# Optimization experiments

Hardware: AMD Instinct MI355X
Metric: run time of the kernel (lower is better)

## Reference

```python
import jax, jax.numpy as jnp
import numpy as np

# Dims: N nodes, C channels (multiplicity), K = 9 input spherical comps (l=0,1,2),
# E elements, output irreps L in {0,1} with M_L = 2L+1, correlation nu = 3.
N, C, K, E = 1024, 128, 9, 10
M = {0: 1, 1: 3}
P = {1: 1, 2: 2, 3: 3}  # number of symmetric-contraction paths per correlation order


def setup_inputs() -> dict:
    key = jax.random.key(0)
    ks = iter(jax.random.split(key, 32))
    inp = {}
    inp["node_feats"] = jax.random.normal(next(ks), (N, C, K), jnp.float32)
    species = jax.random.randint(next(ks), (N,), 0, E)
    inp["node_attrs"] = jax.nn.one_hot(species, E, dtype=jnp.float32)
    inp["sc"] = jax.random.normal(next(ks), (N, C * (M[0] + M[1])), jnp.float32)
    # Generalized CG coefficient tensors U_t (fixed basis; random stand-ins with
    # the same shape/contraction structure as the real Clebsch-Gordan U matrices)
    # and learned element-dependent weights W_t, per output irrep L.
    for L in (0, 1):
        for t in (1, 2, 3):
            u = jax.random.normal(next(ks), (K,) * t + (M[L], P[t]), jnp.float32)
            inp[f"U{t}_{L}"] = u * (K ** (-0.5 * t))
            inp[f"W{t}_{L}"] = jax.random.normal(next(ks), (E, P[t], C), jnp.float32) / np.sqrt(P[t])
        inp[f"Wlin_{L}"] = jax.random.normal(next(ks), (C, C), jnp.float32)
    return inp


def _sym_contract(x, na, U1, U2, U3, W1, W2, W3):
    # x: [N,C,K] node features, na: [N,E] one-hot element attrs.
    # Per-node path weights: [N,P_t,C]
    w1 = jnp.einsum('ne,epc->npc', na, W1)
    w2 = jnp.einsum('ne,epc->npc', na, W2)
    w3 = jnp.einsum('ne,epc->npc', na, W3)
    # Horner-style recursion of MACE's Contraction (highest order first):
    out = jnp.einsum('ijkmp,npc,nck->ncmij', U3, w3, x)      # [N,C,M,K,K]
    ct = jnp.einsum('ijmp,npc->ncmij', U2, w2) + out
    out = jnp.einsum('ncmij,ncj->ncmi', ct, x)               # [N,C,M,K]
    ct = jnp.einsum('imp,npc->ncmi', U1, w1) + out
    out = jnp.einsum('ncmi,nci->ncm', ct, x)                 # [N,C,M]
    return out


def reference(node_feats, node_attrs, sc,
              U1_0, U2_0, U3_0, U1_1, U2_1, U3_1,
              W1_0, W2_0, W3_0, W1_1, W2_1, W3_1,
              Wlin_0, Wlin_1):
    y0 = _sym_contract(node_feats, node_attrs, U1_0, U2_0, U3_0, W1_0, W2_0, W3_0)  # [N,C,1]
    y1 = _sym_contract(node_feats, node_attrs, U1_1, U2_1, U3_1, W1_1, W2_1, W3_1)  # [N,C,3]
    inv = 1.0 / np.sqrt(node_feats.shape[1])  # e3nn Linear fan-in normalization
    z0 = jnp.einsum('ncm,cd->ndm', y0, Wlin_0) * inv
    z1 = jnp.einsum('ncm,cd->ndm', y1, Wlin_1) * inv
    n = node_feats.shape[0]
    out = jnp.concatenate([z0.reshape(n, -1), z1.reshape(n, -1)], axis=-1)  # [N, 512]
    return out + sc
```

## Files before the change

### kernel.cpp

```cpp
#include <hip/hip_runtime.h>


typedef __attribute__((ext_vector_type(8))) short short8;
typedef __attribute__((ext_vector_type(16))) float f32x16;

#define NSTEP 14
#define TBLB_DWORDS (NSTEP*64*4)
#define WL_OFF TBLB_DWORDS
#define TBLW_DWORDS (64*256)

static __device__ __forceinline__ short bf16b(float f) {
  __bf16 h = (__bf16)f;
  return __builtin_bit_cast(short, h);
}

struct Triples { unsigned char a[224], b[224], c3[224], ord[224]; };
constexpr Triples make_triples() {
  Triples T{};
  int s = 0;
  for (int i = 0; i < 9; ++i)
    for (int j = i; j < 9; ++j)
      for (int k = j; k < 9; ++k) { T.a[s]=(unsigned char)i; T.b[s]=(unsigned char)j; T.c3[s]=(unsigned char)k; T.ord[s]=3; ++s; }
  for (int i = 0; i < 9; ++i)
    for (int j = i; j < 9; ++j) { T.a[s]=(unsigned char)i; T.b[s]=(unsigned char)j; T.ord[s]=2; ++s; }
  for (int i = 0; i < 9; ++i) { T.a[s]=(unsigned char)i; T.ord[s]=1; ++s; }
  for (; s < 224; ++s) T.ord[s] = 0;
  return T;
}
static constexpr Triples TRI = make_triples();

struct DecTab {
  unsigned short b3[165][6]; unsigned char c3[165];
  unsigned short b2[45][2];  unsigned char c2[45];
};
constexpr DecTab make_dectab() {
  DecTab D{};
  int s = 0;
  for (int i = 0; i < 9; ++i)
    for (int j = i; j < 9; ++j)
      for (int k = j; k < 9; ++k) {
        int pm[6][3] = {{i,j,k},{i,k,j},{j,i,k},{j,k,i},{k,i,j},{k,j,i}};
        int cnt = 0;
        for (int q = 0; q < 6; ++q) {
          bool dup = false;
          for (int r = 0; r < q; ++r)
            if (pm[r][0]==pm[q][0] && pm[r][1]==pm[q][1] && pm[r][2]==pm[q][2]) dup = true;
          if (!dup) { D.b3[s][cnt] = (unsigned short)((pm[q][0]*9 + pm[q][1])*9 + pm[q][2]); ++cnt; }
        }
        D.c3[s] = (unsigned char)cnt; ++s;
      }
  s = 0;
  for (int i = 0; i < 9; ++i)
    for (int j = i; j < 9; ++j) {
      D.b2[s][0] = (unsigned short)(i*9 + j);
      D.b2[s][1] = (unsigned short)(j*9 + i);
      D.c2[s] = (unsigned char)((i == j) ? 1 : 2); ++s;
    }
  return D;
}
static constexpr DecTab DT = make_dectab();

template<int KI>
static __device__ __forceinline__ float monoT(const float* xr) {
  if constexpr (TRI.ord[KI] == 3) return xr[TRI.a[KI]] * xr[TRI.b[KI]] * xr[TRI.c3[KI]];
  else if constexpr (TRI.ord[KI] == 2) return xr[TRI.a[KI]] * xr[TRI.b[KI]];
  else if constexpr (TRI.ord[KI] == 1) return xr[TRI.a[KI]];
  else return 0.f;
}

template<int K0>
static __device__ __forceinline__ void mono8(const float* xr, float m[8]) {
  m[0]=monoT<K0+0>(xr); m[1]=monoT<K0+1>(xr); m[2]=monoT<K0+2>(xr); m[3]=monoT<K0+3>(xr);
  m[4]=monoT<K0+4>(xr); m[5]=monoT<K0+5>(xr); m[6]=monoT<K0+6>(xr); m[7]=monoT<K0+7>(xr);
}

template<int T>
static __device__ __forceinline__ void k_steps(const float* xr, const unsigned int* __restrict__ tbl,
                                               int lane, int ks, f32x16& acc) {
  if constexpr (T < NSTEP) {
    float m[8];
    if (ks == 0) mono8<T*16>(xr, m);
    else         mono8<T*16 + 8>(xr, m);
    short8 mf;
    mf[0]=bf16b(m[0]); mf[1]=bf16b(m[1]); mf[2]=bf16b(m[2]); mf[3]=bf16b(m[3]);
    mf[4]=bf16b(m[4]); mf[5]=bf16b(m[5]); mf[6]=bf16b(m[6]); mf[7]=bf16b(m[7]);
    short8 cf = *(const short8*)&tbl[(T*64 + lane)*4];
    acc = __builtin_amdgcn_mfma_f32_32x32x16_bf16(cf, mf, acc, 0, 0, 0);
    k_steps<T+1>(xr, tbl, lane, ks, acc);
  }
}

static __device__ __forceinline__ float coefval(int k, int col,
    const float* U1_0, const float* U2_0, const float* U3_0,
    const float* U1_1, const float* U2_1, const float* U3_1) {
  if (k < 165) {
    if (col < 12 || col >= 24) return 0.f;
    int mp = (col - 12) / 3, p = (col - 12) % 3;
    float acc = 0.f;
    int cnt = DT.c3[k];
    for (int q = 0; q < cnt; ++q) {
      int base = DT.b3[k][q];
      acc += (mp == 0) ? U3_0[base*3 + p] : U3_1[base*9 + (mp-1)*3 + p];
    }
    return acc;
  } else if (k < 210) {
    if (col < 4 || col >= 12) return 0.f;
    int mp = (col - 4) / 2, p = (col - 4) % 2;
    int s2 = k - 165;
    float acc = 0.f;
    int cnt = DT.c2[s2];
    for (int q = 0; q < cnt; ++q) {
      int base = DT.b2[s2][q];
      acc += (mp == 0) ? U2_0[base*2 + p] : U2_1[(base*3 + (mp-1))*2 + p];
    }
    return acc;
  } else if (k < 219) {
    int i = k - 210;
    if (col == 0) return U1_0[i];
    if (col < 4) return U1_1[i*3 + (col-1)];
    return 0.f;
  }
  return 0.f;
}

__global__ __launch_bounds__(64) void build_tables_kernel(
    const float* __restrict__ U1_0, const float* __restrict__ U2_0, const float* __restrict__ U3_0,
    const float* __restrict__ U1_1, const float* __restrict__ U2_1, const float* __restrict__ U3_1,
    const float* __restrict__ Wl0, const float* __restrict__ Wl1,
    unsigned int* __restrict__ tbl) {
  const int b = blockIdx.x, l = threadIdx.x;
  const int col = l & 31, ks = l >> 5;
  if (b < NSTEP) {
    const int ft = b;
    #pragma unroll
    for (int d = 0; d < 4; ++d) {
      int k = ft*16 + ks*8 + d*2;
      unsigned short lo = (unsigned short)bf16b(coefval(k,   col, U1_0,U2_0,U3_0,U1_1,U2_1,U3_1));
      unsigned short hi = (unsigned short)bf16b(coefval(k+1, col, U1_0,U2_0,U3_0,U1_1,U2_1,U3_1));
      tbl[(ft*64 + l)*4 + d] = ((unsigned int)hi << 16) | lo;
    }
  } else {
    const int u = b - NSTEP;
    const int g = u >> 5, u5 = u & 31, nt = u5 >> 3, st = u5 & 7;
    const float* W = g ? Wl1 : Wl0;
    #pragma unroll
    for (int d = 0; d < 4; ++d) {
      int k = st*16 + ks*8 + 2*d;
      unsigned short lo = (unsigned short)bf16b(W[(long)k*128     + nt*32 + col]);
      unsigned short hi = (unsigned short)bf16b(W[(long)(k+1)*128 + nt*32 + col]);
      tbl[WL_OFF + u*256 + l*4 + d] = ((unsigned int)hi << 16) | lo;
    }
  }
}

__global__ __launch_bounds__(512, 4) void epbb_mfma_kernel(
    const float* __restrict__ xg,
    const float* __restrict__ na,
    const float* __restrict__ sc,
    const float* __restrict__ W1_0, const float* __restrict__ W2_0, const float* __restrict__ W3_0,
    const float* __restrict__ W1_1, const float* __restrict__ W2_1, const float* __restrict__ W3_1,
    const unsigned int* __restrict__ tbl,
    float* __restrict__ out) {
  __shared__ __align__(16) short lds_yA[2][8][136];

  const int tid  = threadIdx.x;
  const int lane = tid & 63;
  const int w    = tid >> 6;
  const int ks   = lane >> 5;
  const int n0   = blockIdx.x * 2;

  const int nw = w >> 2;
  const int n  = n0 + nw;
  const int c0 = (w & 3) * 32;
  const int cl = c0 + (lane & 31);
  const float* xp = xg + ((long)(n*128 + cl))*9;
  float xr[9];
  #pragma unroll
  for (int q = 0; q < 9; ++q) xr[q] = xp[q];

  int e = 0;
  #pragma unroll
  for (int q = 0; q < 10; ++q) e = (na[(long)n*10 + q] > 0.5f) ? q : e;

  const float w10  = W1_0[e*128 + cl];
  const float w20a = W2_0[(e*2+0)*128 + cl], w20b = W2_0[(e*2+1)*128 + cl];
  const float w30a = W3_0[(e*3+0)*128 + cl], w30b = W3_0[(e*3+1)*128 + cl], w30c = W3_0[(e*3+2)*128 + cl];
  const float w11  = W1_1[e*128 + cl];
  const float w21a = W2_1[(e*2+0)*128 + cl], w21b = W2_1[(e*2+1)*128 + cl];
  const float w31a = W3_1[(e*3+0)*128 + cl], w31b = W3_1[(e*3+1)*128 + cl], w31c = W3_1[(e*3+2)*128 + cl];

  f32x16 acc;
  #pragma unroll
  for (int q = 0; q < 16; ++q) acc[q] = 0.f;

  k_steps<0>(xr, tbl, lane, ks, acc);

  float p0, p1, p2, p3;
  if (ks == 0) {
    p0 = w10*acc[0];
    p1 = w11*acc[1] + w31b*acc[8]  + w31c*acc[9];
    p2 = w11*acc[2] + w21a*acc[4]  + w21b*acc[5] + w31a*acc[10] + w31b*acc[11];
    p3 = w11*acc[3] + w21a*acc[6]  + w21b*acc[7];
  } else {
    p0 = w20a*acc[0] + w20b*acc[1] + w30a*acc[4] + w30b*acc[5] + w30c*acc[6];
    p1 = w21a*acc[2] + w21b*acc[3] + w31a*acc[7];
    p2 = w31c*acc[8];
    p3 = w31a*acc[9] + w31b*acc[10] + w31c*acc[11];
  }
  const float y0 = p0 + __shfl_xor(p0, 32, 64);
  const float y1 = p1 + __shfl_xor(p1, 32, 64);
  const float y2 = p2 + __shfl_xor(p2, 32, 64);
  const float y3 = p3 + __shfl_xor(p3, 32, 64);

  if (ks == 0) {
    lds_yA[0][nw][cl]     = bf16b(y0);
    lds_yA[1][nw][cl]     = bf16b(y1);
  } else {
    lds_yA[1][2 + nw][cl] = bf16b(y2);
    lds_yA[1][4 + nw][cl] = bf16b(y3);
  }
  __syncthreads();

  const int g  = w >> 2;
  const int nt = w & 3;
  f32x16 z;
  #pragma unroll
  for (int q = 0; q < 16; ++q) z[q] = 0.f;
  const unsigned int* bw = tbl + WL_OFF + ((g*4 + nt)*8)*256;
  #pragma unroll
  for (int st = 0; st < 8; ++st) {
    short8 af = *(const short8*)&lds_yA[g][lane & 7][st*16 + ks*8];
    short8 bf = *(const short8*)&bw[st*256 + lane*4];
    z = __builtin_amdgcn_mfma_f32_32x32x16_bf16(af, bf, z, 0, 0, 0);
  }
  const float inv = 0.088388347648318447f;
  const int d = nt*32 + (lane & 31);
  if (g == 0) {
    if (ks == 0) {
      #pragma unroll
      for (int r = 0; r < 2; ++r) {
        long o = (long)(n0 + r)*512 + d;
        out[o] = z[r]*inv + sc[o];
      }
    }
  } else {
    if (ks == 0) {
      #pragma unroll
      for (int r = 0; r < 4; ++r) {
        long o = (long)(n0 + (r & 1))*512 + 128 + 3*d + (r >> 1);
        out[o] = z[r]*inv + sc[o];
      }
    } else {
      #pragma unroll
      for (int r = 0; r < 2; ++r) {
        long o = (long)(n0 + r)*512 + 128 + 3*d + 2;
        out[o] = z[r]*inv + sc[o];
      }
    }
  }
}

extern "C" void kernel_launch(void* const* d_in, const int* in_sizes, int n_in,
                              void* d_out, int out_size, void* d_ws, size_t ws_size,
                              hipStream_t stream) {
  const float* xg   = (const float*)d_in[0];
  const float* na   = (const float*)d_in[1];
  const float* sc   = (const float*)d_in[2];
  const float* U1_0 = (const float*)d_in[3];
  const float* W1_0 = (const float*)d_in[4];
  const float* U2_0 = (const float*)d_in[5];
  const float* W2_0 = (const float*)d_in[6];
  const float* U3_0 = (const float*)d_in[7];
  const float* W3_0 = (const float*)d_in[8];
  const float* Wl0  = (const float*)d_in[9];
  const float* U1_1 = (const float*)d_in[10];
  const float* W1_1 = (const float*)d_in[11];
  const float* U2_1 = (const float*)d_in[12];
  const float* W2_1 = (const float*)d_in[13];
  const float* U3_1 = (const float*)d_in[14];
  const float* W3_1 = (const float*)d_in[15];
  const float* Wl1  = (const float*)d_in[16];

  unsigned int* tbl = (unsigned int*)d_ws;
  const int N = in_sizes[0] / (128 * 9);

  hipLaunchKernelGGL(build_tables_kernel, dim3(NSTEP + 64), dim3(64), 0, stream,
                     U1_0, U2_0, U3_0, U1_1, U2_1, U3_1, Wl0, Wl1, tbl);
  hipLaunchKernelGGL(epbb_mfma_kernel, dim3(N/2), dim3(512), 0, stream,
                     xg, na, sc, W1_0, W2_0, W3_0, W1_1, W2_1, W3_1, tbl,
                     (float*)d_out);
}
```

Baseline: 25.64 us.

## Stage coefficient table and inputs in LDS, coalesce output stores

The coefficient B-table is copied into shared memory once per block, so the MFMA operand loads read LDS instead of global memory. Node features are loaded with coalesced float4 copies into LDS rather than 9 strided scalar loads per thread. The output is gathered in LDS and written together with the sc residual as coalesced float4 stores instead of scattered scalar writes. This adds about 14KB of LDS per block and extra barriers, which may reduce occupancy.

```diff
diff --git a/kernel.cpp b/kernel.cpp
--- a/kernel.cpp
+++ b/kernel.cpp
@@ -75,7 +75,7 @@
 }
 
 template<int T>
-static __device__ __forceinline__ void k_steps(const float* xr, const unsigned int* __restrict__ tbl,
+static __device__ __forceinline__ void k_steps(const float* xr, const unsigned int* lds_b,
                                                int lane, int ks, f32x16& acc) {
   if constexpr (T < NSTEP) {
     float m[8];
@@ -84,9 +84,9 @@
     short8 mf;
     mf[0]=bf16b(m[0]); mf[1]=bf16b(m[1]); mf[2]=bf16b(m[2]); mf[3]=bf16b(m[3]);
     mf[4]=bf16b(m[4]); mf[5]=bf16b(m[5]); mf[6]=bf16b(m[6]); mf[7]=bf16b(m[7]);
-    short8 cf = *(const short8*)&tbl[(T*64 + lane)*4];
+    short8 cf = *(const short8*)&lds_b[(T*64 + lane)*4];
     acc = __builtin_amdgcn_mfma_f32_32x32x16_bf16(cf, mf, acc, 0, 0, 0);
-    k_steps<T+1>(xr, tbl, lane, ks, acc);
+    k_steps<T+1>(xr, lds_b, lane, ks, acc);
   }
 }
 
@@ -161,7 +161,10 @@
     const float* __restrict__ W1_1, const float* __restrict__ W2_1, const float* __restrict__ W3_1,
     const unsigned int* __restrict__ tbl,
     float* __restrict__ out) {
+  __shared__ __align__(16) unsigned int lds_b[TBLB_DWORDS];
+  __shared__ __align__(16) float lds_x[2*128*9];
   __shared__ __align__(16) short lds_yA[2][8][136];
+  __shared__ __align__(16) float lds_out[2*512];
 
   const int tid  = threadIdx.x;
   const int lane = tid & 63;
@@ -169,14 +172,18 @@
   const int ks   = lane >> 5;
   const int n0   = blockIdx.x * 2;
 
+  for (int q = tid; q < TBLB_DWORDS; q += 512) lds_b[q] = tbl[q];
+  {
+    const float4* xg4 = (const float4*)(xg + (long)n0*1152);
+    float4* lx4 = (float4*)lds_x;
+    #pragma unroll
+    for (int q = tid; q < 576; q += 512) lx4[q] = xg4[q];
+  }
+
   const int nw = w >> 2;
   const int n  = n0 + nw;
   const int c0 = (w & 3) * 32;
   const int cl = c0 + (lane & 31);
-  const float* xp = xg + ((long)(n*128 + cl))*9;
-  float xr[9];
-  #pragma unroll
-  for (int q = 0; q < 9; ++q) xr[q] = xp[q];
 
   int e = 0;
   #pragma unroll
@@ -189,11 +196,20 @@
   const float w21a = W2_1[(e*2+0)*128 + cl], w21b = W2_1[(e*2+1)*128 + cl];
   const float w31a = W3_1[(e*3+0)*128 + cl], w31b = W3_1[(e*3+1)*128 + cl], w31c = W3_1[(e*3+2)*128 + cl];
 
+  __syncthreads();
+
+  float xr[9];
+  {
+    const float* myx = lds_x + (nw*128 + cl)*9;
+    #pragma unroll
+    for (int q = 0; q < 9; ++q) xr[q] = myx[q];
+  }
+
   f32x16 acc;
   #pragma unroll
   for (int q = 0; q < 16; ++q) acc[q] = 0.f;
 
-  k_steps<0>(xr, tbl, lane, ks, acc);
+  k_steps<0>(xr, lds_b, lane, ks, acc);
 
   float p0, p1, p2, p3;
   if (ks == 0) {
@@ -237,26 +253,27 @@
   const int d = nt*32 + (lane & 31);
   if (g == 0) {
     if (ks == 0) {
-      #pragma unroll
-      for (int r = 0; r < 2; ++r) {
-        long o = (long)(n0 + r)*512 + d;
-        out[o] = z[r]*inv + sc[o];
-      }
+      lds_out[0*512 + d] = z[0]*inv;
+      lds_out[1*512 + d] = z[1]*inv;
     }
   } else {
     if (ks == 0) {
-      #pragma unroll
-      for (int r = 0; r < 4; ++r) {
-        long o = (long)(n0 + (r & 1))*512 + 128 + 3*d + (r >> 1);
-        out[o] = z[r]*inv + sc[o];
-      }
+      lds_out[0*512 + 128 + 3*d + 0] = z[0]*inv;
+      lds_out[1*512 + 128 + 3*d + 0] = z[1]*inv;
+      lds_out[0*512 + 128 + 3*d + 1] = z[2]*inv;
+      lds_out[1*512 + 128 + 3*d + 1] = z[3]*inv;
     } else {
-      #pragma unroll
-      for (int r = 0; r < 2; ++r) {
-        long o = (long)(n0 + r)*512 + 128 + 3*d + 2;
-        out[o] = z[r]*inv + sc[o];
-      }
-    }
+      lds_out[0*512 + 128 + 3*d + 2] = z[0]*inv;
+      lds_out[1*512 + 128 + 3*d + 2] = z[1]*inv;
+    }
+  }
+  __syncthreads();
+
+  if (tid < 256) {
+    float4 v = ((const float4*)lds_out)[tid];
+    float4 s = *(const float4*)(sc + (long)n0*512 + tid*4);
+    v.x += s.x; v.y += s.y; v.z += s.z; v.w += s.w;
+    *(float4*)(out + (long)n0*512 + tid*4) = v;
   }
 }
 
```

Measured after the change: 25.36 us. About the same (-1.1%).

## Process four nodes per block, stage coefficient table and skip in LDS

Applied to the files above, without the earlier changes.

Each block now handles four nodes instead of two. Each wave computes two 32-channel tiles, so the output linear MFMA runs on fuller A rows (4 or 16 rows instead of 2 or 8). The 14-step coefficient table is copied once into LDS and the MFMA B operands are read from there rather than global memory. The skip tensor is prefetched into LDS with vector loads. This amortises table loads and the linear-layer weights over more nodes, at the cost of more LDS, more registers, lower occupancy bounds and half as many blocks.

```diff
diff --git a/kernel.cpp b/kernel.cpp
--- a/kernel.cpp
+++ b/kernel.cpp
@@ -5,6 +5,7 @@
 typedef __attribute__((ext_vector_type(16))) float f32x16;
 
 #define NSTEP 14
+#define NODES 4
 #define TBLB_DWORDS (NSTEP*64*4)
 #define WL_OFF TBLB_DWORDS
 #define TBLW_DWORDS (64*256)
@@ -75,7 +76,7 @@
 }
 
 template<int T>
-static __device__ __forceinline__ void k_steps(const float* xr, const unsigned int* __restrict__ tbl,
+static __device__ __forceinline__ void k_steps(const float* xr, const unsigned int* lds_b,
                                                int lane, int ks, f32x16& acc) {
   if constexpr (T < NSTEP) {
     float m[8];
@@ -84,9 +85,43 @@
     short8 mf;
     mf[0]=bf16b(m[0]); mf[1]=bf16b(m[1]); mf[2]=bf16b(m[2]); mf[3]=bf16b(m[3]);
     mf[4]=bf16b(m[4]); mf[5]=bf16b(m[5]); mf[6]=bf16b(m[6]); mf[7]=bf16b(m[7]);
-    short8 cf = *(const short8*)&tbl[(T*64 + lane)*4];
+    short8 cf = *(const short8*)&lds_b[(T*64 + lane)*4];
     acc = __builtin_amdgcn_mfma_f32_32x32x16_bf16(cf, mf, acc, 0, 0, 0);
-    k_steps<T+1>(xr, tbl, lane, ks, acc);
+    k_steps<T+1>(xr, lds_b, lane, ks, acc);
+  }
+}
+
+struct PathW { float w10,w20a,w20b,w30a,w30b,w30c,w11,w21a,w21b,w31a,w31b,w31c; };
+
+static __device__ __forceinline__ void process_tile(
+    const float* xr, const PathW& W, const unsigned int* lds_b,
+    short* yA0, short* yA1, int lane, int ks, int nd, int cl) {
+  f32x16 acc;
+  #pragma unroll
+  for (int q = 0; q < 16; ++q) acc[q] = 0.f;
+  k_steps<0>(xr, lds_b, lane, ks, acc);
+  float p0, p1, p2, p3;
+  if (ks == 0) {
+    p0 = W.w10*acc[0];
+    p1 = W.w11*acc[1] + W.w31b*acc[8]  + W.w31c*acc[9];
+    p2 = W.w11*acc[2] + W.w21a*acc[4]  + W.w21b*acc[5] + W.w31a*acc[10] + W.w31b*acc[11];
+    p3 = W.w11*acc[3] + W.w21a*acc[6]  + W.w21b*acc[7];
+  } else {
+    p0 = W.w20a*acc[0] + W.w20b*acc[1] + W.w30a*acc[4] + W.w30b*acc[5] + W.w30c*acc[6];
+    p1 = W.w21a*acc[2] + W.w21b*acc[3] + W.w31a*acc[7];
+    p2 = W.w31c*acc[8];
+    p3 = W.w31a*acc[9] + W.w31b*acc[10] + W.w31c*acc[11];
+  }
+  const float y0 = p0 + __shfl_xor(p0, 32, 64);
+  const float y1 = p1 + __shfl_xor(p1, 32, 64);
+  const float y2 = p2 + __shfl_xor(p2, 32, 64);
+  const float y3 = p3 + __shfl_xor(p3, 32, 64);
+  if (ks == 0) {
+    yA0[nd*136 + cl]       = bf16b(y0);
+    yA1[nd*136 + cl]       = bf16b(y1);
+  } else {
+    yA1[(4+nd)*136 + cl]   = bf16b(y2);
+    yA1[(8+nd)*136 + cl]   = bf16b(y3);
   }
 }
 
@@ -153,7 +188,7 @@
   }
 }
 
-__global__ __launch_bounds__(512, 4) void epbb_mfma_kernel(
+__global__ __launch_bounds__(512, 2) void epbb_mfma_kernel(
     const float* __restrict__ xg,
     const float* __restrict__ na,
     const float* __restrict__ sc,
@@ -161,64 +196,56 @@
     const float* __restrict__ W1_1, const float* __restrict__ W2_1, const float* __restrict__ W3_1,
     const unsigned int* __restrict__ tbl,
     float* __restrict__ out) {
-  __shared__ __align__(16) short lds_yA[2][8][136];
+  __shared__ __align__(16) unsigned int lds_b[TBLB_DWORDS];
+  __shared__ __align__(16) short lds_yA0[4*136];
+  __shared__ __align__(16) short lds_yA1[16*136];
+  __shared__ __align__(16) float lds_sc[NODES*512];
 
   const int tid  = threadIdx.x;
   const int lane = tid & 63;
   const int w    = tid >> 6;
   const int ks   = lane >> 5;
-  const int n0   = blockIdx.x * 2;
-
-  const int nw = w >> 2;
-  const int n  = n0 + nw;
-  const int c0 = (w & 3) * 32;
-  const int cl = c0 + (lane & 31);
-  const float* xp = xg + ((long)(n*128 + cl))*9;
-  float xr[9];
-  #pragma unroll
-  for (int q = 0; q < 9; ++q) xr[q] = xp[q];
+  const int n0   = blockIdx.x * NODES;
+
+  const int nd  = w >> 1;
+  const int n   = n0 + nd;
+  const int cla = (w & 1)*64 + (lane & 31);
+  const int clb = cla + 32;
+
+  float xrA[9], xrB[9];
+  {
+    const float* xpA = xg + ((long)(n*128 + cla))*9;
+    const float* xpB = xg + ((long)(n*128 + clb))*9;
+    #pragma unroll
+    for (int q = 0; q < 9; ++q) { xrA[q] = xpA[q]; xrB[q] = xpB[q]; }
+  }
+
+  for (int q = tid; q < TBLB_DWORDS; q += 512) lds_b[q] = tbl[q];
+  ((float4*)lds_sc)[tid] = ((const float4*)(sc + (long)n0*512))[tid];
 
   int e = 0;
   #pragma unroll
   for (int q = 0; q < 10; ++q) e = (na[(long)n*10 + q] > 0.5f) ? q : e;
 
-  const float w10  = W1_0[e*128 + cl];
-  const float w20a = W2_0[(e*2+0)*128 + cl], w20b = W2_0[(e*2+1)*128 + cl];
-  const float w30a = W3_0[(e*3+0)*128 + cl], w30b = W3_0[(e*3+1)*128 + cl], w30c = W3_0[(e*3+2)*128 + cl];
-  const float w11  = W1_1[e*128 + cl];
-  const float w21a = W2_1[(e*2+0)*128 + cl], w21b = W2_1[(e*2+1)*128 + cl];
-  const float w31a = W3_1[(e*3+0)*128 + cl], w31b = W3_1[(e*3+1)*128 + cl], w31c = W3_1[(e*3+2)*128 + cl];
-
-  f32x16 acc;
-  #pragma unroll
-  for (int q = 0; q < 16; ++q) acc[q] = 0.f;
-
-  k_steps<0>(xr, tbl, lane, ks, acc);
-
-  float p0, p1, p2, p3;
-  if (ks == 0) {
-    p0 = w10*acc[0];
-    p1 = w11*acc[1] + w31b*acc[8]  + w31c*acc[9];
-    p2 = w11*acc[2] + w21a*acc[4]  + w21b*acc[5] + w31a*acc[10] + w31b*acc[11];
-    p3 = w11*acc[3] + w21a*acc[6]  + w21b*acc[7];
-  } else {
-    p0 = w20a*acc[0] + w20b*acc[1] + w30a*acc[4] + w30b*acc[5] + w30c*acc[6];
-    p1 = w21a*acc[2] + w21b*acc[3] + w31a*acc[7];
-    p2 = w31c*acc[8];
-    p3 = w31a*acc[9] + w31b*acc[10] + w31c*acc[11];
-  }
-  const float y0 = p0 + __shfl_xor(p0, 32, 64);
-  const float y1 = p1 + __shfl_xor(p1, 32, 64);
-  const float y2 = p2 + __shfl_xor(p2, 32, 64);
-  const float y3 = p3 + __shfl_xor(p3, 32, 64);
-
-  if (ks == 0) {
-    lds_yA[0][nw][cl]     = bf16b(y0);
-    lds_yA[1][nw][cl]     = bf16b(y1);
-  } else {
-    lds_yA[1][2 + nw][cl] = bf16b(y2);
-    lds_yA[1][4 + nw][cl] = bf16b(y3);
-  }
+  PathW WA, WB;
+  WA.w10  = W1_0[e*128 + cla];              WB.w10  = W1_0[e*128 + clb];
+  WA.w20a = W2_0[(e*2+0)*128 + cla];        WB.w20a = W2_0[(e*2+0)*128 + clb];
+  WA.w20b = W2_0[(e*2+1)*128 + cla];        WB.w20b = W2_0[(e*2+1)*128 + clb];
+  WA.w30a = W3_0[(e*3+0)*128 + cla];        WB.w30a = W3_0[(e*3+0)*128 + clb];
+  WA.w30b = W3_0[(e*3+1)*128 + cla];        WB.w30b = W3_0[(e*3+1)*128 + clb];
+  WA.w30c = W3_0[(e*3+2)*128 + cla];        WB.w30c = W3_0[(e*3+2)*128 + clb];
+  WA.w11  = W1_1[e*128 + cla];              WB.w11  = W1_1[e*128 + clb];
+  WA.w21a = W2_1[(e*2+0)*128 + cla];        WB.w21a = W2_1[(e*2+0)*128 + clb];
+  WA.w21b = W2_1[(e*2+1)*128 + cla];        WB.w21b = W2_1[(e*2+1)*128 + clb];
+  WA.w31a = W3_1[(e*3+0)*128 + cla];        WB.w31a = W3_1[(e*3+0)*128 + clb];
+  WA.w31b = W3_1[(e*3+1)*128 + cla];        WB.w31b = W3_1[(e*3+1)*128 + clb];
+  WA.w31c = W3_1[(e*3+2)*128 + cla];        WB.w31c = W3_1[(e*3+2)*128 + clb];
+
+  __syncthreads();
+
+  process_tile(xrA, WA, lds_b, lds_yA0, lds_yA1, lane, ks, nd, cla);
+  process_tile(xrB, WB, lds_b, lds_yA0, lds_yA1, lane, ks, nd, clb);
+
   __syncthreads();
 
   const int g  = w >> 2;
@@ -227,9 +254,11 @@
   #pragma unroll
   for (int q = 0; q < 16; ++q) z[q] = 0.f;
   const unsigned int* bw = tbl + WL_OFF + ((g*4 + nt)*8)*256;
+  const short* yA = g ? lds_yA1 : lds_yA0;
+  const int arow = g ? (lane & 15) : (lane & 3);
   #pragma unroll
   for (int st = 0; st < 8; ++st) {
-    short8 af = *(const short8*)&lds_yA[g][lane & 7][st*16 + ks*8];
+    short8 af = *(const short8*)&yA[arow*136 + st*16 + ks*8];
     short8 bf = *(const short8*)&bw[st*256 + lane*4];
     z = __builtin_amdgcn_mfma_f32_32x32x16_bf16(af, bf, z, 0, 0, 0);
   }
@@ -238,23 +267,28 @@
   if (g == 0) {
     if (ks == 0) {
       #pragma unroll
-      for (int r = 0; r < 2; ++r) {
+      for (int r = 0; r < 4; ++r) {
         long o = (long)(n0 + r)*512 + d;
-        out[o] = z[r]*inv + sc[o];
+        out[o] = z[r]*inv + lds_sc[r*512 + d];
       }
     }
   } else {
     if (ks == 0) {
       #pragma unroll
       for (int r = 0; r < 4; ++r) {
-        long o = (long)(n0 + (r & 1))*512 + 128 + 3*d + (r >> 1);
-        out[o] = z[r]*inv + sc[o];
+        long o = (long)(n0 + r)*512 + 128 + 3*d + 0;
+        out[o] = z[r]*inv + lds_sc[r*512 + 128 + 3*d + 0];
+      }
+      #pragma unroll
+      for (int r = 4; r < 8; ++r) {
+        long o = (long)(n0 + (r-4))*512 + 128 + 3*d + 2;
+        out[o] = z[r]*inv + lds_sc[(r-4)*512 + 128 + 3*d + 2];
       }
     } else {
       #pragma unroll
-      for (int r = 0; r < 2; ++r) {
-        long o = (long)(n0 + r)*512 + 128 + 3*d + 2;
-        out[o] = z[r]*inv + sc[o];
+      for (int r = 0; r < 4; ++r) {
+        long o = (long)(n0 + r)*512 + 128 + 3*d + 1;
+        out[o] = z[r]*inv + lds_sc[r*512 + 128 + 3*d + 1];
       }
     }
   }
@@ -286,7 +320,7 @@
 
   hipLaunchKernelGGL(build_tables_kernel, dim3(NSTEP + 64), dim3(64), 0, stream,
                      U1_0, U2_0, U3_0, U1_1, U2_1, U3_1, Wl0, Wl1, tbl);
-  hipLaunchKernelGGL(epbb_mfma_kernel, dim3(N/2), dim3(512), 0, stream,
+  hipLaunchKernelGGL(epbb_mfma_kernel, dim3(N/NODES), dim3(512), 0, stream,
                      xg, na, sc, W1_0, W2_0, W3_0, W1_1, W2_1, W3_1, tbl,
                      (float*)d_out);
 }
```

Result: no change. 25.67 us (+0.1%).

## Fuse table build into main kernel with paired monomial packing and precomputed pair products

Applied to the files above, without the earlier changes.

Removes the separate table-building launch. Each block now builds the CG coefficient table in LDS, and the Wlin weights are converted to bf16 from global memory inside the output GEMM loop. Monomials are reordered into pairs that share a quadratic factor, so each MFMA lane reuses precomputed x_i*x_j products (P45) instead of recomputing triple products. In exchange, every one of the 512 blocks redoes the coefficient-table work and Wlin conversion. Register pressure also rises, and the occupancy hint drops from 4 to 2.

```diff
diff --git a/kernel.cpp b/kernel.cpp
--- a/kernel.cpp
+++ b/kernel.cpp
@@ -5,29 +5,68 @@
 typedef __attribute__((ext_vector_type(16))) float f32x16;
 
 #define NSTEP 14
+#define NPOS (NSTEP*8)
 #define TBLB_DWORDS (NSTEP*64*4)
-#define WL_OFF TBLB_DWORDS
-#define TBLW_DWORDS (64*256)
 
 static __device__ __forceinline__ short bf16b(float f) {
   __bf16 h = (__bf16)f;
   return __builtin_bit_cast(short, h);
 }
 
-struct Triples { unsigned char a[224], b[224], c3[224], ord[224]; };
-constexpr Triples make_triples() {
-  Triples T{};
-  int s = 0;
+constexpr int pidx(int i, int j) { return 9*i - i*(i-1)/2 + (j - i); }
+
+struct MonoGF { unsigned char g, f; };
+constexpr MonoGF mono_gf(int id) {
+  if (id < 165) {
+    int s = 0;
+    for (int i = 0; i < 9; ++i)
+      for (int j = i; j < 9; ++j)
+        for (int k = j; k < 9; ++k) {
+          if (s == id) return MonoGF{(unsigned char)pidx(i,j), (unsigned char)k};
+          ++s;
+        }
+  } else if (id < 210) {
+    int s = 165;
+    for (int i = 0; i < 9; ++i)
+      for (int j = i; j < 9; ++j) {
+        if (s == id) return MonoGF{(unsigned char)pidx(i,j), (unsigned char)9};
+        ++s;
+      }
+  } else if (id < 219) {
+    return MonoGF{45, (unsigned char)(id - 210)};
+  }
+  return MonoGF{45, 10};
+}
+
+struct PairTab { short m0[NPOS], m1[NPOS]; };
+constexpr PairTab make_pairtab() {
+  PairTab P{};
+  int pos = 0;
+  short singles3[32]{}; int ns3 = 0;
+  int id = 0;
   for (int i = 0; i < 9; ++i)
-    for (int j = i; j < 9; ++j)
-      for (int k = j; k < 9; ++k) { T.a[s]=(unsigned char)i; T.b[s]=(unsigned char)j; T.c3[s]=(unsigned char)k; T.ord[s]=3; ++s; }
-  for (int i = 0; i < 9; ++i)
-    for (int j = i; j < 9; ++j) { T.a[s]=(unsigned char)i; T.b[s]=(unsigned char)j; T.ord[s]=2; ++s; }
-  for (int i = 0; i < 9; ++i) { T.a[s]=(unsigned char)i; T.ord[s]=1; ++s; }
-  for (; s < 224; ++s) T.ord[s] = 0;
-  return T;
-}
-static constexpr Triples TRI = make_triples();
+    for (int j = i; j < 9; ++j) {
+      int sz = 9 - j;
+      int base = id;
+      int t = 0;
+      for (; t + 1 < sz; t += 2) { P.m0[pos] = (short)(base+t); P.m1[pos] = (short)(base+t+1); ++pos; }
+      if (t < sz) singles3[ns3++] = (short)(base + t);
+      id += sz;
+    }
+  int u = 0;
+  for (; u + 1 < ns3; u += 2) { P.m0[pos] = singles3[u]; P.m1[pos] = singles3[u+1]; ++pos; }
+  short left3 = (u < ns3) ? singles3[u] : (short)-1;
+  int o2 = 165;
+  for (; o2 + 1 < 210; o2 += 2) { P.m0[pos] = (short)o2; P.m1[pos] = (short)(o2+1); ++pos; }
+  short left2 = (o2 < 210) ? (short)o2 : (short)-1;
+  if (left3 >= 0 && left2 >= 0) { P.m0[pos] = left3; P.m1[pos] = left2; ++pos; }
+  int o1 = 210;
+  for (; o1 + 1 < 219; o1 += 2) { P.m0[pos] = (short)o1; P.m1[pos] = (short)(o1+1); ++pos; }
+  P.m0[pos] = 218; P.m1[pos] = 219; ++pos;
+  for (; pos < NPOS; ++pos) { P.m0[pos] = 219; P.m1[pos] = 219; }
+  return P;
+}
+static constexpr PairTab PT = make_pairtab();
 
 struct DecTab {
   unsigned short b3[165][6]; unsigned char c3[165];
@@ -60,53 +99,23 @@
 }
 static constexpr DecTab DT = make_dectab();
 
-template<int KI>
-static __device__ __forceinline__ float monoT(const float* xr) {
-  if constexpr (TRI.ord[KI] == 3) return xr[TRI.a[KI]] * xr[TRI.b[KI]] * xr[TRI.c3[KI]];
-  else if constexpr (TRI.ord[KI] == 2) return xr[TRI.a[KI]] * xr[TRI.b[KI]];
-  else if constexpr (TRI.ord[KI] == 1) return xr[TRI.a[KI]];
-  else return 0.f;
-}
-
-template<int K0>
-static __device__ __forceinline__ void mono8(const float* xr, float m[8]) {
-  m[0]=monoT<K0+0>(xr); m[1]=monoT<K0+1>(xr); m[2]=monoT<K0+2>(xr); m[3]=monoT<K0+3>(xr);
-  m[4]=monoT<K0+4>(xr); m[5]=monoT<K0+5>(xr); m[6]=monoT<K0+6>(xr); m[7]=monoT<K0+7>(xr);
-}
-
-template<int T>
-static __device__ __forceinline__ void k_steps(const float* xr, const unsigned int* __restrict__ tbl,
-                                               int lane, int ks, f32x16& acc) {
-  if constexpr (T < NSTEP) {
-    float m[8];
-    if (ks == 0) mono8<T*16>(xr, m);
-    else         mono8<T*16 + 8>(xr, m);
-    short8 mf;
-    mf[0]=bf16b(m[0]); mf[1]=bf16b(m[1]); mf[2]=bf16b(m[2]); mf[3]=bf16b(m[3]);
-    mf[4]=bf16b(m[4]); mf[5]=bf16b(m[5]); mf[6]=bf16b(m[6]); mf[7]=bf16b(m[7]);
-    short8 cf = *(const short8*)&tbl[(T*64 + lane)*4];
-    acc = __builtin_amdgcn_mfma_f32_32x32x16_bf16(cf, mf, acc, 0, 0, 0);
-    k_steps<T+1>(xr, tbl, lane, ks, acc);
-  }
-}
-
-static __device__ __forceinline__ float coefval(int k, int col,
+static __device__ __forceinline__ float coefval(int id, int col,
     const float* U1_0, const float* U2_0, const float* U3_0,
     const float* U1_1, const float* U2_1, const float* U3_1) {
-  if (k < 165) {
+  if (id < 165) {
     if (col < 12 || col >= 24) return 0.f;
     int mp = (col - 12) / 3, p = (col - 12) % 3;
     float acc = 0.f;
-    int cnt = DT.c3[k];
+    int cnt = DT.c3[id];
     for (int q = 0; q < cnt; ++q) {
-      int base = DT.b3[k][q];
+      int base = DT.b3[id][q];
       acc += (mp == 0) ? U3_0[base*3 + p] : U3_1[base*9 + (mp-1)*3 + p];
     }
     return acc;
-  } else if (k < 210) {
+  } else if (id < 210) {
     if (col < 4 || col >= 12) return 0.f;
     int mp = (col - 4) / 2, p = (col - 4) % 2;
-    int s2 = k - 165;
+    int s2 = id - 165;
     float acc = 0.f;
     int cnt = DT.c2[s2];
     for (int q = 0; q < cnt; ++q) {
@@ -114,8 +123,8 @@
       acc += (mp == 0) ? U2_0[base*2 + p] : U2_1[(base*3 + (mp-1))*2 + p];
     }
     return acc;
-  } else if (k < 219) {
-    int i = k - 210;
+  } else if (id < 219) {
+    int i = id - 210;
     if (col == 0) return U1_0[i];
     if (col < 4) return U1_1[i*3 + (col-1)];
     return 0.f;
@@ -123,56 +132,81 @@
   return 0.f;
 }
 
-__global__ __launch_bounds__(64) void build_tables_kernel(
-    const float* __restrict__ U1_0, const float* __restrict__ U2_0, const float* __restrict__ U3_0,
-    const float* __restrict__ U1_1, const float* __restrict__ U2_1, const float* __restrict__ U3_1,
-    const float* __restrict__ Wl0, const float* __restrict__ Wl1,
-    unsigned int* __restrict__ tbl) {
-  const int b = blockIdx.x, l = threadIdx.x;
-  const int col = l & 31, ks = l >> 5;
-  if (b < NSTEP) {
-    const int ft = b;
-    #pragma unroll
-    for (int d = 0; d < 4; ++d) {
-      int k = ft*16 + ks*8 + d*2;
-      unsigned short lo = (unsigned short)bf16b(coefval(k,   col, U1_0,U2_0,U3_0,U1_1,U2_1,U3_1));
-      unsigned short hi = (unsigned short)bf16b(coefval(k+1, col, U1_0,U2_0,U3_0,U1_1,U2_1,U3_1));
-      tbl[(ft*64 + l)*4 + d] = ((unsigned int)hi << 16) | lo;
-    }
+template<int POS>
+static __device__ __forceinline__ float monoPos(const float* P45, const float* xr, bool ks1) {
+  constexpr MonoGF A = mono_gf(PT.m0[POS]);
+  constexpr MonoGF B = mono_gf(PT.m1[POS]);
+  if constexpr (A.f == 10 && B.f == 10) {
+    return 0.0f;
+  } else if constexpr (B.f == 10) {
+    float va = (A.g == 45) ? 1.0f : P45[A.g];
+    if constexpr (A.f != 9) va *= xr[A.f];
+    return ks1 ? 0.0f : va;
+  } else if constexpr (A.f == 10) {
+    float vb = (B.g == 45) ? 1.0f : P45[B.g];
+    if constexpr (B.f != 9) vb *= xr[B.f];
+    return ks1 ? vb : 0.0f;
   } else {
-    const int u = b - NSTEP;
-    const int g = u >> 5, u5 = u & 31, nt = u5 >> 3, st = u5 & 7;
-    const float* W = g ? Wl1 : Wl0;
-    #pragma unroll
-    for (int d = 0; d < 4; ++d) {
-      int k = st*16 + ks*8 + 2*d;
-      unsigned short lo = (unsigned short)bf16b(W[(long)k*128     + nt*32 + col]);
-      unsigned short hi = (unsigned short)bf16b(W[(long)(k+1)*128 + nt*32 + col]);
-      tbl[WL_OFF + u*256 + l*4 + d] = ((unsigned int)hi << 16) | lo;
-    }
-  }
-}
-
-__global__ __launch_bounds__(512, 4) void epbb_mfma_kernel(
+    float gv;
+    if constexpr (A.g == B.g) gv = (A.g == 45) ? 1.0f : P45[A.g];
+    else {
+      float ga = (A.g == 45) ? 1.0f : P45[A.g];
+      float gb = (B.g == 45) ? 1.0f : P45[B.g];
+      gv = ks1 ? gb : ga;
+    }
+    if constexpr (A.f == 9 && B.f == 9) return gv;
+    else if constexpr (A.f == B.f) return gv * xr[A.f];
+    else {
+      float fa = (A.f == 9) ? 1.0f : xr[A.f];
+      float fb = (B.f == 9) ? 1.0f : xr[B.f];
+      return gv * (ks1 ? fb : fa);
+    }
+  }
+}
+
+template<int T>
+static __device__ __forceinline__ void k_steps(const float* P45, const float* xr, bool ks1,
+                                               const unsigned int* lds_b, int lane, f32x16& acc) {
+  if constexpr (T < NSTEP) {
+    float m[8];
+    m[0]=monoPos<T*8+0>(P45,xr,ks1); m[1]=monoPos<T*8+1>(P45,xr,ks1);
+    m[2]=monoPos<T*8+2>(P45,xr,ks1); m[3]=monoPos<T*8+3>(P45,xr,ks1);
+    m[4]=monoPos<T*8+4>(P45,xr,ks1); m[5]=monoPos<T*8+5>(P45,xr,ks1);
+    m[6]=monoPos<T*8+6>(P45,xr,ks1); m[7]=monoPos<T*8+7>(P45,xr,ks1);
+    short8 mf;
+    mf[0]=bf16b(m[0]); mf[1]=bf16b(m[1]); mf[2]=bf16b(m[2]); mf[3]=bf16b(m[3]);
+    mf[4]=bf16b(m[4]); mf[5]=bf16b(m[5]); mf[6]=bf16b(m[6]); mf[7]=bf16b(m[7]);
+    short8 cf = *(const short8*)&lds_b[(T*64 + lane)*4];
+    acc = __builtin_amdgcn_mfma_f32_32x32x16_bf16(cf, mf, acc, 0, 0, 0);
+    k_steps<T+1>(P45, xr, ks1, lds_b, lane, acc);
+  }
+}
+
+__global__ __launch_bounds__(512, 2) void epbb_mfma_kernel(
     const float* __restrict__ xg,
     const float* __restrict__ na,
     const float* __restrict__ sc,
+    const float* __restrict__ U1_0, const float* __restrict__ U2_0, const float* __restrict__ U3_0,
+    const float* __restrict__ U1_1, const float* __restrict__ U2_1, const float* __restrict__ U3_1,
     const float* __restrict__ W1_0, const float* __restrict__ W2_0, const float* __restrict__ W3_0,
     const float* __restrict__ W1_1, const float* __restrict__ W2_1, const float* __restrict__ W3_1,
-    const unsigned int* __restrict__ tbl,
+    const float* __restrict__ Wlin0, const float* __restrict__ Wlin1,
     float* __restrict__ out) {
+  __shared__ __align__(16) unsigned int lds_b[TBLB_DWORDS];
   __shared__ __align__(16) short lds_yA[2][8][136];
 
   const int tid  = threadIdx.x;
   const int lane = tid & 63;
   const int w    = tid >> 6;
   const int ks   = lane >> 5;
+  const bool ks1 = (ks != 0);
   const int n0   = blockIdx.x * 2;
 
   const int nw = w >> 2;
   const int n  = n0 + nw;
   const int c0 = (w & 3) * 32;
   const int cl = c0 + (lane & 31);
+
   const float* xp = xg + ((long)(n*128 + cl))*9;
   float xr[9];
   #pragma unroll
@@ -181,7 +215,6 @@
   int e = 0;
   #pragma unroll
   for (int q = 0; q < 10; ++q) e = (na[(long)n*10 + q] > 0.5f) ? q : e;
-
   const float w10  = W1_0[e*128 + cl];
   const float w20a = W2_0[(e*2+0)*128 + cl], w20b = W2_0[(e*2+1)*128 + cl];
   const float w30a = W3_0[(e*3+0)*128 + cl], w30b = W3_0[(e*3+1)*128 + cl], w30c = W3_0[(e*3+2)*128 + cl];
@@ -189,11 +222,35 @@
   const float w21a = W2_1[(e*2+0)*128 + cl], w21b = W2_1[(e*2+1)*128 + cl];
   const float w31a = W3_1[(e*3+0)*128 + cl], w31b = W3_1[(e*3+1)*128 + cl], w31c = W3_1[(e*3+2)*128 + cl];
 
+  for (int q = tid; q < TBLB_DWORDS; q += 512) {
+    int l    = (q >> 2) & 63;
+    int d    = q & 3;
+    int ft   = q >> 8;
+    int col  = l & 31;
+    int ksb  = l >> 5;
+    int pos0 = ft*8 + 2*d;
+    int id0  = ksb ? PT.m1[pos0]     : PT.m0[pos0];
+    int id1  = ksb ? PT.m1[pos0 + 1] : PT.m0[pos0 + 1];
+    unsigned short lo = (unsigned short)bf16b(coefval(id0, col, U1_0,U2_0,U3_0,U1_1,U2_1,U3_1));
+    unsigned short hi = (unsigned short)bf16b(coefval(id1, col, U1_0,U2_0,U3_0,U1_1,U2_1,U3_1));
+    lds_b[q] = ((unsigned int)hi << 16) | lo;
+  }
+
+  float P45[45];
+  {
+    int s = 0;
+    #pragma unroll
+    for (int i = 0; i < 9; ++i)
+      #pragma unroll
+      for (int j = i; j < 9; ++j) { P45[s] = xr[i]*xr[j]; ++s; }
+  }
+
   f32x16 acc;
   #pragma unroll
   for (int q = 0; q < 16; ++q) acc[q] = 0.f;
 
-  k_steps<0>(xr, tbl, lane, ks, acc);
+  __syncthreads();
+  k_steps<0>(P45, xr, ks1, lds_b, lane, acc);
 
   float p0, p1, p2, p3;
   if (ks == 0) {
@@ -223,15 +280,24 @@
 
   const int g  = w >> 2;
   const int nt = w & 3;
+  const float* Wl = g ? Wlin1 : Wlin0;
+  const int colw = nt*32 + (lane & 31);
   f32x16 z;
   #pragma unroll
   for (int q = 0; q < 16; ++q) z[q] = 0.f;
-  const unsigned int* bw = tbl + WL_OFF + ((g*4 + nt)*8)*256;
   #pragma unroll
   for (int st = 0; st < 8; ++st) {
     short8 af = *(const short8*)&lds_yA[g][lane & 7][st*16 + ks*8];
-    short8 bf = *(const short8*)&bw[st*256 + lane*4];
-    z = __builtin_amdgcn_mfma_f32_32x32x16_bf16(af, bf, z, 0, 0, 0);
+    unsigned int bw[4];
+    #pragma unroll
+    for (int d2 = 0; d2 < 4; ++d2) {
+      int k0 = st*16 + ks*8 + 2*d2;
+      unsigned short lo = (unsigned short)bf16b(Wl[(long)k0*128 + colw]);
+      unsigned short hi = (unsigned short)bf16b(Wl[(long)(k0+1)*128 + colw]);
+      bw[d2] = ((unsigned int)hi << 16) | lo;
+    }
+    short8 bfv = __builtin_bit_cast(short8, *(uint4*)bw);
+    z = __builtin_amdgcn_mfma_f32_32x32x16_bf16(af, bfv, z, 0, 0, 0);
   }
   const float inv = 0.088388347648318447f;
   const int d = nt*32 + (lane & 31);
@@ -280,13 +346,12 @@
   const float* U3_1 = (const float*)d_in[14];
   const float* W3_1 = (const float*)d_in[15];
   const float* Wl1  = (const float*)d_in[16];
-
-  unsigned int* tbl = (unsigned int*)d_ws;
+  (void)d_ws; (void)ws_size; (void)n_in; (void)out_size;
+
   const int N = in_sizes[0] / (128 * 9);
 
-  hipLaunchKernelGGL(build_tables_kernel, dim3(NSTEP + 64), dim3(64), 0, stream,
-                     U1_0, U2_0, U3_0, U1_1, U2_1, U3_1, Wl0, Wl1, tbl);
   hipLaunchKernelGGL(epbb_mfma_kernel, dim3(N/2), dim3(512), 0, stream,
-                     xg, na, sc, W1_0, W2_0, W3_0, W1_1, W2_1, W3_1, tbl,
+                     xg, na, sc, U1_0, U2_0, U3_0, U1_1, U2_1, U3_1,
+                     W1_0, W2_0, W3_0, W1_1, W2_1, W3_1, Wl0, Wl1,
                      (float*)d_out);
 }
```

Result: slower. 29.27 us (+14.2%).
